# Kernel tuning notes

Hardware: AMD Instinct MI355X
Metric: run time of the kernel (lower is better)

The kernel has to match this reference:

```python
import jax, jax.numpy as jnp
import numpy as np

N, B, F, H = 100000, 128, 512, 256


def setup_inputs() -> dict:
    key = jax.random.key(0)
    ks = jax.random.split(key, 9)
    pos = jax.random.normal(ks[0], (N, 3), dtype=jnp.float32)
    mass_center = jax.random.normal(ks[1], (B, 3), dtype=jnp.float32)
    scaler = jax.random.normal(ks[2], (N, F), dtype=jnp.float32)
    vector = jax.random.normal(ks[3], (N, 3), dtype=jnp.float32)
    batch_index = jax.random.randint(ks[4], (N,), 0, B, dtype=jnp.int64)
    # MLP params (Linear(F,H) -> act -> Linear(H,1)), kaiming-uniform-ish init
    lim1 = 1.0 / np.sqrt(F)
    lim2 = 1.0 / np.sqrt(H)
    W1 = jax.random.uniform(ks[5], (F, H), minval=-lim1, maxval=lim1, dtype=jnp.float32)
    b1 = jax.random.uniform(ks[6], (H,), minval=-lim1, maxval=lim1, dtype=jnp.float32)
    W2 = jax.random.uniform(ks[7], (H, 1), minval=-lim2, maxval=lim2, dtype=jnp.float32)
    b2 = jax.random.uniform(ks[8], (1,), minval=-lim2, maxval=lim2, dtype=jnp.float32)
    return {"pos": pos, "mass_center": mass_center, "scaler": scaler,
            "vector": vector, "batch_index": batch_index,
            "W1": W1, "b1": b1, "W2": W2, "b2": b2}


def reference(pos, mass_center, scaler, vector, batch_index, W1, b1, W2, b2):
    # gather per-graph mass center to nodes: [N,3]
    mass_center_vec = pos - mass_center[batch_index]
    # tiny 2-layer MLP on node scalars: [N,F] -> [N,H] -> [N,1]
    h = jax.nn.silu(scaler @ W1 + b1)
    q_i = h @ W2 + b2                         # [N,1]
    # squared L2 norm of displacement: [N,1]
    r2_i = jnp.sum(mass_center_vec * mass_center_vec, axis=1, keepdims=True)
    # scatter-sum per graph: [B,1]
    out = jax.ops.segment_sum(q_i * r2_i, batch_index, num_segments=B)
    return out
```

## Files before the change

### kernel.cpp

```cpp
#include <hip/hip_runtime.h>
#include <hip/hip_bf16.h>
#include <stdint.h>

#define F_DIM 512
#define H_DIM 256
#define B_DIM 128
#define M_BLK 128
#define NCHUNK 16
#define NBUF 2

typedef __bf16 bf16x8 __attribute__((ext_vector_type(8)));
typedef float  f32x4  __attribute__((ext_vector_type(4)));

__global__ __launch_bounds__(256) void convert_w1_kernel(
    const float* __restrict__ W1, __bf16* __restrict__ W1t) {
    int t = blockIdx.x * 256 + threadIdx.x;
    int c = t >> 9;
    int k = t & 511;
    W1t[t] = (__bf16)W1[k * H_DIM + c];
}

__device__ inline void gload_lds16(const float* g, float* lds) {
    __builtin_amdgcn_global_load_lds(
        (const __attribute__((address_space(1))) uint32_t*)g,
        (__attribute__((address_space(3))) uint32_t*)lds, 16, 0, 0);
}
__device__ inline void gload_lds16b(const __bf16* g, __bf16* lds) {
    __builtin_amdgcn_global_load_lds(
        (const __attribute__((address_space(1))) uint32_t*)g,
        (__attribute__((address_space(3))) uint32_t*)lds, 16, 0, 0);
}

__device__ inline int bswz(int col) { return (col & 3) ^ ((col >> 2) & 3); }

template<bool USE_PARTIAL>
__global__ __launch_bounds__(1024) void fused_mlp_kernel(
    const float* __restrict__ pos,
    const float* __restrict__ mass_center,
    const float* __restrict__ scaler,
    const int*   __restrict__ batch_index,
    const __bf16* __restrict__ W1t,
    const float* __restrict__ b1,
    const float* __restrict__ W2,
    const float* __restrict__ b2,
    float* __restrict__ outp,
    int N)
{
    __shared__ float  A_lds[NBUF][M_BLK][32];
    __shared__ __bf16 Bc_lds[NBUF][H_DIM][32];
    __shared__ float  q_lds[M_BLK];
    __shared__ float  pb[B_DIM];

    const int tid    = threadIdx.x;
    const int lane   = tid & 63;
    const int wid    = tid >> 6;
    const int wave_m = wid >> 2;
    const int wave_n = wid & 3;
    const int lrow   = lane & 15;
    const int kq     = (lane >> 4) * 8;
    const int row_base = blockIdx.x * M_BLK;

    if (tid < M_BLK) q_lds[tid] = 0.f;
    if (USE_PARTIAL && tid < B_DIM) pb[tid] = 0.f;

    const int srow = tid >> 3;
    const int sseg = (tid & 7) ^ (srow & 7);
    int grA = row_base + srow; if (grA >= N) grA = N - 1;
    const float* gsA = scaler + (size_t)grA * F_DIM + sseg * 4;

    const int c0 = tid >> 2;
    const int g0 = (tid & 3) ^ bswz(c0);
    const __bf16* gsB = W1t + (size_t)c0 * F_DIM + g0 * 8;

#define STAGE(buf, c) do {                                                 \
        gload_lds16 (gsA + (c) * 32, &A_lds[(buf)][0][0]  + wid * 256);    \
        gload_lds16b(gsB + (c) * 32, &Bc_lds[(buf)][0][0] + wid * 512);    \
    } while (0)

    f32x4 acc[2][4];
    #pragma unroll
    for (int mi = 0; mi < 2; ++mi)
        #pragma unroll
        for (int ni = 0; ni < 4; ++ni)
            acc[mi][ni] = (f32x4){0.f, 0.f, 0.f, 0.f};

    STAGE(0, 0);
    STAGE(1, 1);

    #pragma unroll
    for (int kc = 0; kc < NCHUNK; ++kc) {
        if (kc < NCHUNK - 1) asm volatile("s_waitcnt vmcnt(2)" ::: "memory");
        else                 asm volatile("s_waitcnt vmcnt(0)" ::: "memory");
        __builtin_amdgcn_s_barrier();

        const int buf = kc & 1;
        bf16x8 af[2];
        #pragma unroll
        for (int mi = 0; mi < 2; ++mi) {
            const int rA = wave_m * 32 + mi * 16 + lrow;
            const int sw = (rA & 7) << 4;
            const char* rb = (const char*)&A_lds[buf][0][0] + rA * 128;
            f32x4 a0 = *(const f32x4*)(rb + ((kq * 4) ^ sw));
            f32x4 a1 = *(const f32x4*)(rb + ((kq * 4 + 16) ^ sw));
            #pragma unroll
            for (int j = 0; j < 4; ++j) {
                af[mi][j]     = (__bf16)a0[j];
                af[mi][4 + j] = (__bf16)a1[j];
            }
        }
        bf16x8 bfrag[4];
        #pragma unroll
        for (int ni = 0; ni < 4; ++ni) {
            const int col = wave_n * 64 + ni * 16 + lrow;
            const int ps  = (lane >> 4) ^ bswz(col);
            bfrag[ni] = *(const bf16x8*)((const char*)&Bc_lds[buf][0][0]
                                         + col * 64 + ps * 16);
        }
        #pragma unroll
        for (int mi = 0; mi < 2; ++mi)
            #pragma unroll
            for (int ni = 0; ni < 4; ++ni)
                acc[mi][ni] = __builtin_amdgcn_mfma_f32_16x16x32_bf16(
                    af[mi], bfrag[ni], acc[mi][ni], 0, 0, 0);

        __builtin_amdgcn_s_barrier();
        if (kc + 2 < NCHUNK)
            STAGE(buf, kc + 2);
    }
#undef STAGE

    float qp[2][4];
    #pragma unroll
    for (int mi = 0; mi < 2; ++mi)
        #pragma unroll
        for (int r = 0; r < 4; ++r) qp[mi][r] = 0.f;

    #pragma unroll
    for (int ni = 0; ni < 4; ++ni) {
        int c = wave_n * 64 + ni * 16 + lrow;
        float b1c = b1[c];
        float w2c = W2[c];
        #pragma unroll
        for (int mi = 0; mi < 2; ++mi)
            #pragma unroll
            for (int r = 0; r < 4; ++r) {
                float h = acc[mi][ni][r] + b1c;
                float s = h / (1.0f + __expf(-h));
                qp[mi][r] += s * w2c;
            }
    }
    #pragma unroll
    for (int off = 1; off < 16; off <<= 1)
        #pragma unroll
        for (int mi = 0; mi < 2; ++mi)
            #pragma unroll
            for (int r = 0; r < 4; ++r)
                qp[mi][r] += __shfl_xor(qp[mi][r], off, 64);

    if ((lane & 15) == 0) {
        int rgrp = lane >> 4;
        #pragma unroll
        for (int mi = 0; mi < 2; ++mi)
            #pragma unroll
            for (int r = 0; r < 4; ++r)
                atomicAdd(&q_lds[wave_m * 32 + mi * 16 + rgrp * 4 + r], qp[mi][r]);
    }
    __syncthreads();

    if (tid < M_BLK) {
        int grow = row_base + tid;
        if (grow < N) {
            float q  = q_lds[tid] + b2[0];
            int   bi = batch_index[grow];
            float dx = pos[grow * 3 + 0] - mass_center[bi * 3 + 0];
            float dy = pos[grow * 3 + 1] - mass_center[bi * 3 + 1];
            float dz = pos[grow * 3 + 2] - mass_center[bi * 3 + 2];
            float val = q * (dx * dx + dy * dy + dz * dz);
            if (USE_PARTIAL) atomicAdd(&pb[bi], val);
            else             atomicAdd(&outp[bi], val);
        }
    }
    if (USE_PARTIAL) {
        __syncthreads();
        if (tid < B_DIM)
            outp[(size_t)blockIdx.x * B_DIM + tid] = pb[tid];
    }
}

__global__ __launch_bounds__(256) void reduce_partials_kernel(
    const float* __restrict__ partial, float* __restrict__ out, int nblk) {
    int b = blockIdx.x;
    float s = 0.f;
    for (int i = threadIdx.x; i < nblk; i += 256)
        s += partial[(size_t)i * B_DIM + b];
    #pragma unroll
    for (int off = 1; off < 64; off <<= 1)
        s += __shfl_xor(s, off, 64);
    __shared__ float wsum[4];
    if ((threadIdx.x & 63) == 0) wsum[threadIdx.x >> 6] = s;
    __syncthreads();
    if (threadIdx.x == 0)
        out[b] = wsum[0] + wsum[1] + wsum[2] + wsum[3];
}

extern "C" void kernel_launch(void* const* d_in, const int* in_sizes, int n_in,
                              void* d_out, int out_size, void* d_ws, size_t ws_size,
                              hipStream_t stream) {
    const float* pos         = (const float*)d_in[0];
    const float* mass_center = (const float*)d_in[1];
    const float* scaler      = (const float*)d_in[2];
    const int*   batch_index = (const int*)d_in[4];
    const float* W1          = (const float*)d_in[5];
    const float* b1          = (const float*)d_in[6];
    const float* W2          = (const float*)d_in[7];
    const float* b2          = (const float*)d_in[8];
    float* out = (float*)d_out;
    (void)n_in; (void)out_size;

    int N = in_sizes[0] / 3;
    int nblk = (N + M_BLK - 1) / M_BLK;

    size_t w1t_bytes  = (size_t)F_DIM * H_DIM * sizeof(__bf16);
    size_t part_bytes = (size_t)nblk * B_DIM * sizeof(float);

    __bf16* W1t = (__bf16*)d_ws;
    convert_w1_kernel<<<(F_DIM * H_DIM) / 256, 256, 0, stream>>>(W1, W1t);

    if (ws_size >= w1t_bytes + part_bytes) {
        float* partial = (float*)((char*)d_ws + w1t_bytes);
        fused_mlp_kernel<true><<<nblk, 1024, 0, stream>>>(
            pos, mass_center, scaler, batch_index, W1t, b1, W2, b2, partial, N);
        reduce_partials_kernel<<<B_DIM, 256, 0, stream>>>(partial, out, nblk);
    } else {
        hipMemsetAsync(out, 0, B_DIM * sizeof(float), stream);
        fused_mlp_kernel<false><<<nblk, 1024, 0, stream>>>(
            pos, mass_center, scaler, batch_index, W1t, b1, W2, b2, out, N);
    }
}
```

Baseline: 88.18 us.

## Shrink GEMM block to 4 waves with 64x128 per-wave tiles

Cuts the fused MLP block from 16 waves to 4. Each wave now computes a 64x128 output tile (4x8 MFMA accumulators) instead of 32x64, which raises fragment reuse per LDS read, and each thread issues four async global-to-LDS loads per stage. It also raises wave priority around the MFMA burst with s_setprio. The cost is much higher register pressure (128 accumulator floats per lane), which may reduce occupancy. Fewer waves are also left to hide load latency.

```diff
diff --git a/kernel.cpp b/kernel.cpp
--- a/kernel.cpp
+++ b/kernel.cpp
@@ -34,7 +34,7 @@
 __device__ inline int bswz(int col) { return (col & 3) ^ ((col >> 2) & 3); }
 
 template<bool USE_PARTIAL>
-__global__ __launch_bounds__(1024) void fused_mlp_kernel(
+__global__ __launch_bounds__(256) void fused_mlp_kernel(
     const float* __restrict__ pos,
     const float* __restrict__ mass_center,
     const float* __restrict__ scaler,
@@ -54,8 +54,8 @@
     const int tid    = threadIdx.x;
     const int lane   = tid & 63;
     const int wid    = tid >> 6;
-    const int wave_m = wid >> 2;
-    const int wave_n = wid & 3;
+    const int wave_m = wid >> 1;
+    const int wave_n = wid & 1;
     const int lrow   = lane & 15;
     const int kq     = (lane >> 4) * 8;
     const int row_base = blockIdx.x * M_BLK;
@@ -63,25 +63,36 @@
     if (tid < M_BLK) q_lds[tid] = 0.f;
     if (USE_PARTIAL && tid < B_DIM) pb[tid] = 0.f;
 
-    const int srow = tid >> 3;
-    const int sseg = (tid & 7) ^ (srow & 7);
-    int grA = row_base + srow; if (grA >= N) grA = N - 1;
-    const float* gsA = scaler + (size_t)grA * F_DIM + sseg * 4;
-
-    const int c0 = tid >> 2;
-    const int g0 = (tid & 3) ^ bswz(c0);
-    const __bf16* gsB = W1t + (size_t)c0 * F_DIM + g0 * 8;
-
-#define STAGE(buf, c) do {                                                 \
-        gload_lds16 (gsA + (c) * 32, &A_lds[(buf)][0][0]  + wid * 256);    \
-        gload_lds16b(gsB + (c) * 32, &Bc_lds[(buf)][0][0] + wid * 512);    \
+    const float* gsA[4];
+    const __bf16* gsB[4];
+    #pragma unroll
+    for (int p = 0; p < 4; ++p) {
+        int sA   = p * 256 + tid;
+        int rowA = sA >> 3;
+        int segA = (sA & 7) ^ (rowA & 7);
+        int grA  = row_base + rowA; if (grA >= N) grA = N - 1;
+        gsA[p] = scaler + (size_t)grA * F_DIM + segA * 4;
+        int sB   = p * 256 + tid;
+        int colB = sB >> 2;
+        int segB = (sB & 3) ^ bswz(colB);
+        gsB[p] = W1t + (size_t)colB * F_DIM + segB * 8;
+    }
+
+#define STAGE(buf, c) do {                                                    \
+        _Pragma("unroll")                                                     \
+        for (int p = 0; p < 4; ++p) {                                         \
+            gload_lds16 (gsA[p] + (c) * 32,                                   \
+                         &A_lds[(buf)][0][0] + p * 1024 + wid * 256);         \
+            gload_lds16b(gsB[p] + (c) * 32,                                   \
+                         &Bc_lds[(buf)][0][0] + p * 2048 + wid * 512);        \
+        }                                                                     \
     } while (0)
 
-    f32x4 acc[2][4];
-    #pragma unroll
-    for (int mi = 0; mi < 2; ++mi)
-        #pragma unroll
-        for (int ni = 0; ni < 4; ++ni)
+    f32x4 acc[4][8];
+    #pragma unroll
+    for (int mi = 0; mi < 4; ++mi)
+        #pragma unroll
+        for (int ni = 0; ni < 8; ++ni)
             acc[mi][ni] = (f32x4){0.f, 0.f, 0.f, 0.f};
 
     STAGE(0, 0);
@@ -89,15 +100,15 @@
 
     #pragma unroll
     for (int kc = 0; kc < NCHUNK; ++kc) {
-        if (kc < NCHUNK - 1) asm volatile("s_waitcnt vmcnt(2)" ::: "memory");
+        if (kc < NCHUNK - 1) asm volatile("s_waitcnt vmcnt(8)" ::: "memory");
         else                 asm volatile("s_waitcnt vmcnt(0)" ::: "memory");
         __builtin_amdgcn_s_barrier();
 
         const int buf = kc & 1;
-        bf16x8 af[2];
-        #pragma unroll
-        for (int mi = 0; mi < 2; ++mi) {
-            const int rA = wave_m * 32 + mi * 16 + lrow;
+        bf16x8 af[4];
+        #pragma unroll
+        for (int mi = 0; mi < 4; ++mi) {
+            const int rA = wave_m * 64 + mi * 16 + lrow;
             const int sw = (rA & 7) << 4;
             const char* rb = (const char*)&A_lds[buf][0][0] + rA * 128;
             f32x4 a0 = *(const f32x4*)(rb + ((kq * 4) ^ sw));
@@ -108,20 +119,22 @@
                 af[mi][4 + j] = (__bf16)a1[j];
             }
         }
-        bf16x8 bfrag[4];
-        #pragma unroll
-        for (int ni = 0; ni < 4; ++ni) {
-            const int col = wave_n * 64 + ni * 16 + lrow;
+        bf16x8 bfrag[8];
+        #pragma unroll
+        for (int ni = 0; ni < 8; ++ni) {
+            const int col = wave_n * 128 + ni * 16 + lrow;
             const int ps  = (lane >> 4) ^ bswz(col);
             bfrag[ni] = *(const bf16x8*)((const char*)&Bc_lds[buf][0][0]
                                          + col * 64 + ps * 16);
         }
-        #pragma unroll
-        for (int mi = 0; mi < 2; ++mi)
-            #pragma unroll
-            for (int ni = 0; ni < 4; ++ni)
+        __builtin_amdgcn_s_setprio(1);
+        #pragma unroll
+        for (int mi = 0; mi < 4; ++mi)
+            #pragma unroll
+            for (int ni = 0; ni < 8; ++ni)
                 acc[mi][ni] = __builtin_amdgcn_mfma_f32_16x16x32_bf16(
                     af[mi], bfrag[ni], acc[mi][ni], 0, 0, 0);
+        __builtin_amdgcn_s_setprio(0);
 
         __builtin_amdgcn_s_barrier();
         if (kc + 2 < NCHUNK)
@@ -129,19 +142,19 @@
     }
 #undef STAGE
 
-    float qp[2][4];
-    #pragma unroll
-    for (int mi = 0; mi < 2; ++mi)
+    float qp[4][4];
+    #pragma unroll
+    for (int mi = 0; mi < 4; ++mi)
         #pragma unroll
         for (int r = 0; r < 4; ++r) qp[mi][r] = 0.f;
 
     #pragma unroll
-    for (int ni = 0; ni < 4; ++ni) {
-        int c = wave_n * 64 + ni * 16 + lrow;
+    for (int ni = 0; ni < 8; ++ni) {
+        int c = wave_n * 128 + ni * 16 + lrow;
         float b1c = b1[c];
         float w2c = W2[c];
         #pragma unroll
-        for (int mi = 0; mi < 2; ++mi)
+        for (int mi = 0; mi < 4; ++mi)
             #pragma unroll
             for (int r = 0; r < 4; ++r) {
                 float h = acc[mi][ni][r] + b1c;
@@ -152,7 +165,7 @@
     #pragma unroll
     for (int off = 1; off < 16; off <<= 1)
         #pragma unroll
-        for (int mi = 0; mi < 2; ++mi)
+        for (int mi = 0; mi < 4; ++mi)
             #pragma unroll
             for (int r = 0; r < 4; ++r)
                 qp[mi][r] += __shfl_xor(qp[mi][r], off, 64);
@@ -160,10 +173,10 @@
     if ((lane & 15) == 0) {
         int rgrp = lane >> 4;
         #pragma unroll
-        for (int mi = 0; mi < 2; ++mi)
+        for (int mi = 0; mi < 4; ++mi)
             #pragma unroll
             for (int r = 0; r < 4; ++r)
-                atomicAdd(&q_lds[wave_m * 32 + mi * 16 + rgrp * 4 + r], qp[mi][r]);
+                atomicAdd(&q_lds[wave_m * 64 + mi * 16 + rgrp * 4 + r], qp[mi][r]);
     }
     __syncthreads();
 
@@ -228,12 +241,12 @@
 
     if (ws_size >= w1t_bytes + part_bytes) {
         float* partial = (float*)((char*)d_ws + w1t_bytes);
-        fused_mlp_kernel<true><<<nblk, 1024, 0, stream>>>(
+        fused_mlp_kernel<true><<<nblk, 256, 0, stream>>>(
             pos, mass_center, scaler, batch_index, W1t, b1, W2, b2, partial, N);
         reduce_partials_kernel<<<B_DIM, 256, 0, stream>>>(partial, out, nblk);
     } else {
         hipMemsetAsync(out, 0, B_DIM * sizeof(float), stream);
-        fused_mlp_kernel<false><<<nblk, 1024, 0, stream>>>(
+        fused_mlp_kernel<false><<<nblk, 256, 0, stream>>>(
             pos, mass_center, scaler, batch_index, W1t, b1, W2, b2, out, N);
     }
 }
```

New measurement: 98.91 us. +12.2%, slower.
